# Kernel optimization log

Measured on AMD Instinct MI355X. Metric: run time of the kernel, lower is better.

The kernel has to match this reference:

```python
import jax, jax.numpy as jnp
import numpy as np

B, N = 16, 64
ATTR, STATE, REL, G = 4, 16, 9, 32
NF = 256  # nf_particle = nf_relation = nf_effect


def _mk_params(key):
    ks = jax.random.split(key, 16)
    s = 0.05
    p = {
        'enc_w0': jax.random.normal(ks[0], (ATTR + STATE, NF)) * s,
        'enc_b0': jnp.zeros((NF,)),
        'enc_w1': jax.random.normal(ks[1], (NF, NF)) * s,
        'enc_b1': jnp.zeros((NF,)),
        'rel_w0': jax.random.normal(ks[2], (REL + STATE + 2 * ATTR, NF)) * s,
        'rel_b0': jnp.zeros((NF,)),
        'rel_w1': jax.random.normal(ks[3], (NF, NF)) * s,
        'rel_b1': jnp.zeros((NF,)),
        'rp_w': jax.random.normal(ks[4], (NF + 2 * NF, NF)) * s,
        'rp_b': jnp.zeros((NF,)),
        'pp_w': jax.random.normal(ks[5], (2 * NF, NF)) * s,
        'pp_b': jnp.zeros((NF,)),
        'pred_w0': jax.random.normal(ks[6], (NF, NF)) * s,
        'pred_b0': jnp.zeros((NF,)),
        'pred_w1': jax.random.normal(ks[7], (NF, G)) * s,
        'pred_b1': jnp.zeros((G,)),
    }
    return p


def setup_inputs() -> dict:
    key = jax.random.key(0)
    k1, k2, k3, k4 = jax.random.split(key, 4)
    inp = {
        'attrs': jax.random.normal(k1, (B, N, ATTR), dtype=jnp.float32),
        'states': jax.random.normal(k2, (B, N, STATE), dtype=jnp.float32),
        'rel_attrs': jax.random.uniform(k3, (B, N, N, REL), dtype=jnp.float32),
        'pstep': 2,
    }
    inp.update(_mk_params(k4))
    return inp


def reference(attrs, states, rel_attrs,
              enc_w0, enc_b0, enc_w1, enc_b1,
              rel_w0, rel_b0, rel_w1, rel_b1,
              rp_w, rp_b, pp_w, pp_b,
              pred_w0, pred_b0, pred_w1, pred_b1,
              pstep):
    relu = jax.nn.relu
    b, n = attrs.shape[0], attrs.shape[1]

    # particle (object) encoder: ReLU(Linear) -> ReLU(Linear)
    obj_in = jnp.concatenate([attrs, states], axis=-1)          # B,N,attr+state
    obj = relu(relu(obj_in @ enc_w0 + enc_b0) @ enc_w1 + enc_b1)  # B,N,NF

    # relation encoder inputs: rel_attrs, pairwise state diffs, recv/send attrs
    rel_states = states[:, :, None, :] - states[:, None, :, :]   # B,N,N,state
    recv_attr = jnp.broadcast_to(attrs[:, :, None, :], (b, n, n, attrs.shape[-1]))
    send_attr = jnp.broadcast_to(attrs[:, None, :, :], (b, n, n, attrs.shape[-1]))
    rel_in = jnp.concatenate([rel_attrs, rel_states, recv_attr, send_attr], axis=-1)
    rel_enc = relu(relu(rel_in @ rel_w0 + rel_b0) @ rel_w1 + rel_b1)  # B,N,N,NF

    # propagation steps (small fixed count; loop over pstep is structural)
    for _ in range(pstep):
        recv = jnp.broadcast_to(obj[:, :, None, :], (b, n, n, obj.shape[-1]))
        send = jnp.broadcast_to(obj[:, None, :, :], (b, n, n, obj.shape[-1]))
        rel_eff = relu(jnp.concatenate([rel_enc, recv, send], axis=-1) @ rp_w + rp_b)
        agg = rel_eff.sum(axis=2)                                 # B,N,NF
        obj = relu(jnp.concatenate([obj, agg], axis=-1) @ pp_w + pp_b)

    # particle predictor + tanh (state encoder variant)
    out = jnp.tanh(relu(obj @ pred_w0 + pred_b0) @ pred_w1 + pred_b1)  # B,N,G
    return out
```

## Files before the change

kernel.cpp:

```cpp
#include <hip/hip_runtime.h>
#include <hip/hip_bf16.h>
#include <math.h>

#define BB 16
#define NN 64
#define ATTR 4
#define STATE 16
#define RELD 9
#define GG 32
#define NF 256
#define NROWS_OBJ (BB*NN)
#define NROWS_REL (BB*NN*NN)

typedef _Float16 half8 __attribute__((ext_vector_type(8)));
typedef _Float16 half4 __attribute__((ext_vector_type(4)));
typedef float  floatx4 __attribute__((ext_vector_type(4)));
typedef unsigned short ushort_t;

__device__ __forceinline__ void split2h(float x, _Float16& h, _Float16& l) {
  h = (_Float16)x;
  l = (_Float16)(x - (float)h);
}

#define F0_ELEMS (2 * 16 * 64 * 8)
#define F1_ELEMS (8 * 16 * 64 * 8)
#define F_TOTAL  (F0_ELEMS + 2 * F1_ELEMS)

__device__ __forceinline__ float4 gemm4_k64(const float* __restrict__ W,
                                            const float* A,
                                            int kseg, int rsel, int c4)
{
  float4 p = make_float4(0.f, 0.f, 0.f, 0.f);
  int k0 = kseg * 64;
#pragma unroll 8
  for (int k = 0; k < 64; ++k) {
    float4 w = *(const float4*)(W + (size_t)(k0 + k) * NF + c4);
    float a = A[rsel * NF + k0 + k];
    p.x += a * w.x; p.y += a * w.y; p.z += a * w.z; p.w += a * w.w;
  }
  return p;
}

__global__ __launch_bounds__(1024) void enc_qr_prep_kernel(
    const float* __restrict__ attrs, const float* __restrict__ states,
    const float* __restrict__ w0, const float* __restrict__ b0,
    const float* __restrict__ w1, const float* __restrict__ b1,
    const float* __restrict__ rpw, const float* __restrict__ rpb,
    const float* __restrict__ rel_w0, const float* __restrict__ rel_w1,
    _Float16* __restrict__ F0, _Float16* __restrict__ F1,
    _Float16* __restrict__ F2,
    float* __restrict__ obj, float* __restrict__ Q, float* __restrict__ R)
{
  int tid = threadIdx.x;
  for (int idx = blockIdx.x * 1024 + tid; idx < F_TOTAL; idx += 256 * 1024) {
    if (idx < F0_ELEMS) {
      int j = idx & 7, lane = (idx >> 3) & 63, g = (idx >> 9) & 15, s = idx >> 13;
      int k = s * 32 + (lane >> 4) * 8 + j, n = g * 16 + (lane & 15);
      float v = (k < 33) ? rel_w0[k * NF + n] : 0.f;
      F0[idx] = (_Float16)v;
    } else if (idx < F0_ELEMS + F1_ELEMS) {
      int t = idx - F0_ELEMS;
      int j = t & 7, lane = (t >> 3) & 63, g = (t >> 9) & 15, s = t >> 13;
      int k = s * 32 + (lane >> 4) * 8 + j, n = g * 16 + (lane & 15);
      F1[t] = (_Float16)rel_w1[k * NF + n];
    } else {
      int t = idx - (F0_ELEMS + F1_ELEMS);
      int j = t & 7, lane = (t >> 3) & 63, g = (t >> 9) & 15, s = t >> 13;
      int k = s * 32 + (lane >> 4) * 8 + j, n = g * 16 + (lane & 15);
      F2[t] = (_Float16)rpw[k * NF + n];
    }
  }
  __shared__ float X[4 * 20];
  __shared__ float H[4 * NF];
  __shared__ float O[4 * NF];
  __shared__ __align__(16) float red[16 * NF];
  int row0 = blockIdx.x * 4;
  if (tid < 80) {
    int r = tid / 20, k = tid % 20;
    int m = row0 + r;
    X[tid] = (k < ATTR) ? attrs[m * ATTR + k] : states[m * STATE + (k - ATTR)];
  }
  __syncthreads();
  int r = tid >> 8, c = tid & 255;
  int kseg = tid >> 8, rsel = (tid >> 6) & 3, c4 = (tid & 63) * 4;
  {
    float a = b0[c];
#pragma unroll
    for (int k = 0; k < 20; ++k) a += X[r * 20 + k] * w0[k * NF + c];
    H[r * NF + c] = fmaxf(a, 0.f);
  }
  __syncthreads();
  {
    float4 p = gemm4_k64(w1, H, kseg, rsel, c4);
    *(float4*)(&red[(kseg * 4 + rsel) * NF + c4]) = p;
  }
  __syncthreads();
  {
    float a = b1[c] + red[(0 + r) * NF + c] + red[(4 + r) * NF + c]
            + red[(8 + r) * NF + c] + red[(12 + r) * NF + c];
    a = fmaxf(a, 0.f);
    O[r * NF + c] = a;
    obj[(row0 + r) * NF + c] = a;
  }
  __syncthreads();
  {
    int gs = tid >> 9, ks2 = (tid >> 8) & 1;
    const float* W = gs ? (rpw + 512 * NF) : (rpw + 256 * NF);
    float4 p = gemm4_k64(W, O, ks2 * 2, rsel, c4);
    float4 q = gemm4_k64(W, O, ks2 * 2 + 1, rsel, c4);
    p.x += q.x; p.y += q.y; p.z += q.z; p.w += q.w;
    *(float4*)(&red[((gs * 2 + ks2) * 4 + rsel) * NF + c4]) = p;
  }
  __syncthreads();
  Q[(row0 + r) * NF + c] = rpb[c] + red[(0 + r) * NF + c] + red[(4 + r) * NF + c];
  R[(row0 + r) * NF + c] = red[(8 + r) * NF + c] + red[(12 + r) * NF + c];
}

#define ROWS 32
#define NRT 2
#define HSTR 264
#define XSTR 72

__global__ __launch_bounds__(256, 4) void rel_agg_store_mfma(
    const float* __restrict__ attrs, const float* __restrict__ states,
    const float* __restrict__ rel_attrs,
    const _Float16* __restrict__ F0, const float* __restrict__ b0,
    const _Float16* __restrict__ F1, const float* __restrict__ b1,
    const _Float16* __restrict__ F2,
    const float* __restrict__ Q, const float* __restrict__ R,
    _Float16* __restrict__ P, float* __restrict__ part)
{
  __shared__ __align__(16) _Float16 S[2 * ROWS * HSTR];
  _Float16* Hh = S;
  _Float16* Hl = S + ROWS * HSTR;
  _Float16* Xh = Hh;
  _Float16* Xl = Hl;

  int tid  = threadIdx.x;
  int wave = tid >> 6;
  int lane = tid & 63;
  int quad = lane >> 4;
  int l16  = lane & 15;
  int row0 = blockIdx.x * ROWS;

  for (int idx = tid; idx < ROWS * 64; idx += 256) {
    int r = idx >> 6, k = idx & 63;
    int grow = row0 + r;
    int j = grow & 63, i = (grow >> 6) & 63, b = grow >> 12;
    float v = 0.f;
    if (k < RELD)                     v = rel_attrs[(size_t)grow * RELD + k];
    else if (k < RELD + STATE)        v = states[(b * NN + i) * STATE + (k - RELD)]
                                        - states[(b * NN + j) * STATE + (k - RELD)];
    else if (k < RELD + STATE + ATTR) v = attrs[(b * NN + i) * ATTR + (k - RELD - STATE)];
    else if (k < 33)                  v = attrs[(b * NN + j) * ATTR + (k - RELD - STATE - ATTR)];
    _Float16 h, l; split2h(v, h, l);
    Xh[r * XSTR + k] = h;
    Xl[r * XSTR + k] = l;
  }
  __syncthreads();

  floatx4 acc[NRT][4];

#define ZERO_ACC() do { \
  _Pragma("unroll") for (int rt = 0; rt < NRT; ++rt) \
  _Pragma("unroll") for (int ct = 0; ct < 4; ++ct) acc[rt][ct] = (floatx4)(0.f); } while (0)

#define STAGE(Sn, AH, AL, ASTR, BF) do { \
  half8 ah[2][NRT], al[2][NRT], bf[2][4]; \
  _Pragma("unroll") for (int ct = 0; ct < 4; ++ct) \
    bf[0][ct] = *(const half8*)((BF) + (size_t)((wave * 4 + ct) * 64 + lane) * 8); \
  _Pragma("unroll") for (int rt = 0; rt < NRT; ++rt) { \
    ah[0][rt] = *(const half8*)(&(AH)[(rt * 16 + l16) * (ASTR) + quad * 8]); \
    al[0][rt] = *(const half8*)(&(AL)[(rt * 16 + l16) * (ASTR) + quad * 8]); } \
  _Pragma("unroll") \
  for (int s = 0; s < (Sn); ++s) { \
    int cur = s & 1, nxt = cur ^ 1; \
    if (s + 1 < (Sn)) { \
      _Pragma("unroll") for (int ct = 0; ct < 4; ++ct) \
        bf[nxt][ct] = *(const half8*)((BF) + (size_t)(((s + 1) * 16 + wave * 4 + ct) * 64 + lane) * 8); \
      _Pragma("unroll") for (int rt = 0; rt < NRT; ++rt) { \
        ah[nxt][rt] = *(const half8*)(&(AH)[(rt * 16 + l16) * (ASTR) + (s + 1) * 32 + quad * 8]); \
        al[nxt][rt] = *(const half8*)(&(AL)[(rt * 16 + l16) * (ASTR) + (s + 1) * 32 + quad * 8]); } } \
    _Pragma("unroll") for (int rt = 0; rt < NRT; ++rt) \
    _Pragma("unroll") for (int ct = 0; ct < 4; ++ct) { \
      acc[rt][ct] = __builtin_amdgcn_mfma_f32_16x16x32_f16(ah[cur][rt], bf[cur][ct], acc[rt][ct], 0, 0, 0); \
      acc[rt][ct] = __builtin_amdgcn_mfma_f32_16x16x32_f16(al[cur][rt], bf[cur][ct], acc[rt][ct], 0, 0, 0); } \
  } } while (0)

  ZERO_ACC();
  STAGE(2, Xh, Xl, XSTR, F0);
  __syncthreads();
#pragma unroll
  for (int ct = 0; ct < 4; ++ct) {
    int col = wave * 64 + ct * 16 + l16;
    float bias = b0[col];
#pragma unroll
    for (int rt = 0; rt < NRT; ++rt)
#pragma unroll
      for (int r = 0; r < 4; ++r) {
        int row = rt * 16 + quad * 4 + r;
        float h = fmaxf(acc[rt][ct][r] + bias, 0.f);
        split2h(h, Hh[row * HSTR + col], Hl[row * HSTR + col]);
      }
  }
  __syncthreads();

  ZERO_ACC();
  STAGE(8, Hh, Hl, HSTR, F1);
  __syncthreads();
#pragma unroll
  for (int ct = 0; ct < 4; ++ct) {
    int col = wave * 64 + ct * 16 + l16;
    float bias = b1[col];
#pragma unroll
    for (int rt = 0; rt < NRT; ++rt)
#pragma unroll
      for (int r = 0; r < 4; ++r) {
        int row = rt * 16 + quad * 4 + r;
        float e = fmaxf(acc[rt][ct][r] + bias, 0.f);
        split2h(e, Hh[row * HSTR + col], Hl[row * HSTR + col]);
      }
  }
  __syncthreads();

  ZERO_ACC();
  STAGE(8, Hh, Hl, HSTR, F2);

#pragma unroll
  for (int ct = 0; ct < 4; ++ct) {
    int col = wave * 64 + ct * 16 + l16;
#pragma unroll
    for (int rt = 0; rt < NRT; ++rt)
#pragma unroll
      for (int r = 0; r < 4; ++r) {
        int row = rt * 16 + quad * 4 + r;
        P[(size_t)(row0 + row) * NF + col] = (_Float16)acc[rt][ct][r];
      }
  }
  __syncthreads();

  {
    float* Rs = (float*)S;
    int bi    = row0 >> 6;
    int jbase = row0 & 63;
    int b     = row0 >> 12;
    for (int idx = tid; idx < ROWS * NF; idx += 256) {
      int rr = idx >> 8, cc = idx & 255;
      Rs[idx] = R[(size_t)(b * NN + jbase + rr) * NF + cc];
    }
    __syncthreads();
#pragma unroll
    for (int ct = 0; ct < 4; ++ct) {
      int col = wave * 64 + ct * 16 + l16;
      float q = Q[bi * NF + col];
      float s = 0.f;
#pragma unroll
      for (int rt = 0; rt < NRT; ++rt)
#pragma unroll
        for (int r = 0; r < 4; ++r) {
          int row = rt * 16 + quad * 4 + r;
          s += fmaxf(acc[rt][ct][r] + q + Rs[row * NF + col], 0.f);
        }
      s += __shfl_xor(s, 16, 64);
      s += __shfl_xor(s, 32, 64);
      if (quad == 0)
        part[((size_t)bi * 2 + (jbase >> 5)) * NF + col] = s;
    }
  }
#undef ZERO_ACC
#undef STAGE
}

__global__ __launch_bounds__(1024) void upd_qr_kernel(
    const float* __restrict__ part, const float* __restrict__ obj,
    const float* __restrict__ ppw, const float* __restrict__ ppb,
    const float* __restrict__ rpw, const float* __restrict__ rpb,
    float* __restrict__ obj_out, float* __restrict__ Qo, float* __restrict__ Ro)
{
  __shared__ float A[4 * NF];
  __shared__ float G[4 * NF];
  __shared__ __align__(16) float red[16 * NF];
  int tid = threadIdx.x;
  int row0 = blockIdx.x * 4;
  int r = tid >> 8, c = tid & 255;
  int kseg = tid >> 8, rsel = (tid >> 6) & 3, c4 = (tid & 63) * 4;
  A[r * NF + c] = obj[(row0 + r) * NF + c];
  G[r * NF + c] = part[((size_t)(row0 + r) * 2 + 0) * NF + c]
                + part[((size_t)(row0 + r) * 2 + 1) * NF + c];
  __syncthreads();
  {
    float4 p = gemm4_k64(ppw, A, kseg, rsel, c4);
    float4 q = gemm4_k64(ppw + NF * NF, G, kseg, rsel, c4);
    p.x += q.x; p.y += q.y; p.z += q.z; p.w += q.w;
    *(float4*)(&red[(kseg * 4 + rsel) * NF + c4]) = p;
  }
  __syncthreads();
  {
    float a = ppb[c] + red[(0 + r) * NF + c] + red[(4 + r) * NF + c]
            + red[(8 + r) * NF + c] + red[(12 + r) * NF + c];
    float o = fmaxf(a, 0.f);
    A[r * NF + c] = o;
    obj_out[(row0 + r) * NF + c] = o;
  }
  __syncthreads();
  {
    int gs = tid >> 9, ks2 = (tid >> 8) & 1;
    const float* W = gs ? (rpw + 512 * NF) : (rpw + 256 * NF);
    float4 p = gemm4_k64(W, A, ks2 * 2, rsel, c4);
    float4 q = gemm4_k64(W, A, ks2 * 2 + 1, rsel, c4);
    p.x += q.x; p.y += q.y; p.z += q.z; p.w += q.w;
    *(float4*)(&red[((gs * 2 + ks2) * 4 + rsel) * NF + c4]) = p;
  }
  __syncthreads();
  Qo[(row0 + r) * NF + c] = rpb[c] + red[(0 + r) * NF + c] + red[(4 + r) * NF + c];
  Ro[(row0 + r) * NF + c] = red[(8 + r) * NF + c] + red[(12 + r) * NF + c];
}

__global__ __launch_bounds__(1024) void aggupd_pred_kernel(
    const _Float16* __restrict__ P, const float* __restrict__ Q,
    const float* __restrict__ R, const float* __restrict__ obj,
    const float* __restrict__ ppw, const float* __restrict__ ppb,
    const float* __restrict__ w0, const float* __restrict__ b0,
    const float* __restrict__ w1, const float* __restrict__ b1,
    float* __restrict__ out)
{
  __shared__ float A[4 * NF];
  __shared__ float G[4 * NF];
  __shared__ __align__(16) float red[16 * NF];
  int tid = threadIdx.x;
  int row0 = blockIdx.x * 4;
  int b = row0 >> 6;
  int r = tid >> 8, c = tid & 255;
  int kseg = tid >> 8, rsel = (tid >> 6) & 3, c4 = (tid & 63) * 4;
  {
    int rr = (tid >> 6) & 3;
    int jq = tid >> 8;
    float4 q4 = *(const float4*)(Q + (row0 + rr) * NF + c4);
    const _Float16* Pb = P + ((size_t)(row0 + rr) * NN + jq * 16) * NF + c4;
    const float* Rb = R + (size_t)(b * NN + jq * 16) * NF + c4;
    float4 s = make_float4(0.f, 0.f, 0.f, 0.f);
#pragma unroll
    for (int j = 0; j < 16; ++j) {
      half4 ph  = *(const half4*)(Pb + (size_t)j * NF);
      float4 rv = *(const float4*)(Rb + (size_t)j * NF);
      s.x += fmaxf((float)ph[0] + q4.x + rv.x, 0.f);
      s.y += fmaxf((float)ph[1] + q4.y + rv.y, 0.f);
      s.z += fmaxf((float)ph[2] + q4.z + rv.z, 0.f);
      s.w += fmaxf((float)ph[3] + q4.w + rv.w, 0.f);
    }
    *(float4*)(&red[(jq * 4 + rr) * NF + c4]) = s;
    A[r * NF + c] = obj[(row0 + r) * NF + c];
  }
  __syncthreads();
  G[r * NF + c] = red[(0 + r) * NF + c] + red[(4 + r) * NF + c]
                + red[(8 + r) * NF + c] + red[(12 + r) * NF + c];
  __syncthreads();
  {
    float4 p = gemm4_k64(ppw, A, kseg, rsel, c4);
    float4 q = gemm4_k64(ppw + NF * NF, G, kseg, rsel, c4);
    p.x += q.x; p.y += q.y; p.z += q.z; p.w += q.w;
    *(float4*)(&red[(kseg * 4 + rsel) * NF + c4]) = p;
  }
  __syncthreads();
  {
    float a = ppb[c] + red[(0 + r) * NF + c] + red[(4 + r) * NF + c]
            + red[(8 + r) * NF + c] + red[(12 + r) * NF + c];
    A[r * NF + c] = fmaxf(a, 0.f);
  }
  __syncthreads();
  {
    float4 p = gemm4_k64(w0, A, kseg, rsel, c4);
    *(float4*)(&red[(kseg * 4 + rsel) * NF + c4]) = p;
  }
  __syncthreads();
  {
    float a = b0[c] + red[(0 + r) * NF + c] + red[(4 + r) * NF + c]
            + red[(8 + r) * NF + c] + red[(12 + r) * NF + c];
    G[r * NF + c] = fmaxf(a, 0.f);
  }
  __syncthreads();
  {
    int ks8 = tid >> 7, rr = (tid >> 5) & 3, g = tid & 31;
    float s = 0.f;
#pragma unroll 8
    for (int k = 0; k < 32; ++k)
      s += G[rr * NF + ks8 * 32 + k] * w1[(ks8 * 32 + k) * GG + g];
    red[tid] = s;
  }
  __syncthreads();
  if (tid < 4 * GG) {
    int rr = tid >> 5, g = tid & 31;
    float a = b1[g];
#pragma unroll
    for (int ks = 0; ks < 8; ++ks) a += red[ks * 128 + tid];
    out[(row0 + rr) * GG + g] = tanhf(a);
  }
}

extern "C" void kernel_launch(void* const* d_in, const int* in_sizes, int n_in,
                              void* d_out, int out_size, void* d_ws, size_t ws_size,
                              hipStream_t stream)
{
  const float* attrs     = (const float*)d_in[0];
  const float* states    = (const float*)d_in[1];
  const float* rel_attrs = (const float*)d_in[2];
  const float* enc_w0  = (const float*)d_in[4];
  const float* enc_b0  = (const float*)d_in[5];
  const float* enc_w1  = (const float*)d_in[6];
  const float* enc_b1  = (const float*)d_in[7];
  const float* rel_w0  = (const float*)d_in[8];
  const float* rel_b0  = (const float*)d_in[9];
  const float* rel_w1  = (const float*)d_in[10];
  const float* rel_b1  = (const float*)d_in[11];
  const float* rp_w    = (const float*)d_in[12];
  const float* rp_b    = (const float*)d_in[13];
  const float* pp_w    = (const float*)d_in[14];
  const float* pp_b    = (const float*)d_in[15];
  const float* pred_w0 = (const float*)d_in[16];
  const float* pred_b0 = (const float*)d_in[17];
  const float* pred_w1 = (const float*)d_in[18];
  const float* pred_b1 = (const float*)d_in[19];
  float* out = (float*)d_out;

  char* ws = (char*)d_ws;
  _Float16* P  = (_Float16*)ws;
  float* obj0  = (float*)(ws + (size_t)NROWS_REL * NF * sizeof(_Float16));
  float* obj1  = obj0 + NROWS_OBJ * NF;
  float* Q0    = obj1 + NROWS_OBJ * NF;
  float* R0    = Q0 + NROWS_OBJ * NF;
  float* Q1    = R0 + NROWS_OBJ * NF;
  float* R1    = Q1 + NROWS_OBJ * NF;
  float* part1 = R1 + NROWS_OBJ * NF;
  _Float16* F0 = (_Float16*)(part1 + 2 * (size_t)NROWS_OBJ * NF);
  _Float16* F1 = F0 + F0_ELEMS;
  _Float16* F2 = F1 + F1_ELEMS;

  enc_qr_prep_kernel<<<NROWS_OBJ / 4, 1024, 0, stream>>>(
      attrs, states, enc_w0, enc_b0, enc_w1, enc_b1, rp_w, rp_b,
      rel_w0, rel_w1, F0, F1, F2, obj0, Q0, R0);
  rel_agg_store_mfma<<<NROWS_REL / ROWS, 256, 0, stream>>>(
      attrs, states, rel_attrs,
      F0, rel_b0, F1, rel_b1, F2,
      Q0, R0, P, part1);
  upd_qr_kernel<<<NROWS_OBJ / 4, 1024, 0, stream>>>(part1, obj0, pp_w, pp_b,
                                                    rp_w, rp_b, obj1, Q1, R1);
  aggupd_pred_kernel<<<NROWS_OBJ / 4, 1024, 0, stream>>>(P, Q1, R1, obj1,
                                                         pp_w, pp_b,
                                                         pred_w0, pred_b0,
                                                         pred_w1, pred_b1, out);
}
```

Before: 231.2 us.

## Swizzle hidden-activation LDS layout to drop padding and raise occupancy

Removes the row padding from the shared hidden-activation buffer (stride 264 to 256) and applies an XOR swizzle on the column index so that MFMA operand reads and epilogue writes stay free of bank conflicts. The smaller LDS footprint supports raising the launch bound from 4 to 5 blocks per SM. It also wraps the MFMA issue block in s_setprio to favour matrix instructions among competing waves. The risk is register pressure under the tighter launch bound, which could cause spills, and any other code that reads the hidden buffer must use the same swizzle.

```diff
diff --git a/kernel.cpp b/kernel.cpp
--- a/kernel.cpp
+++ b/kernel.cpp
@@ -118,10 +118,14 @@
 
 #define ROWS 32
 #define NRT 2
-#define HSTR 264
+#define HSTR 256
 #define XSTR 72
 
-__global__ __launch_bounds__(256, 4) void rel_agg_store_mfma(
+__device__ __forceinline__ int hsw(int row, int col) {
+  return ((row << 8) + col) ^ (((row >> 1) & 7) << 3);
+}
+
+__global__ __launch_bounds__(256, 5) void rel_agg_store_mfma(
     const float* __restrict__ attrs, const float* __restrict__ states,
     const float* __restrict__ rel_attrs,
     const _Float16* __restrict__ F0, const float* __restrict__ b0,
@@ -165,13 +169,15 @@
   _Pragma("unroll") for (int rt = 0; rt < NRT; ++rt) \
   _Pragma("unroll") for (int ct = 0; ct < 4; ++ct) acc[rt][ct] = (floatx4)(0.f); } while (0)
 
-#define STAGE(Sn, AH, AL, ASTR, BF) do { \
+#define STAGE(Sn, AH, AL, ASTR, SW, BF) do { \
   half8 ah[2][NRT], al[2][NRT], bf[2][4]; \
   _Pragma("unroll") for (int ct = 0; ct < 4; ++ct) \
     bf[0][ct] = *(const half8*)((BF) + (size_t)((wave * 4 + ct) * 64 + lane) * 8); \
   _Pragma("unroll") for (int rt = 0; rt < NRT; ++rt) { \
-    ah[0][rt] = *(const half8*)(&(AH)[(rt * 16 + l16) * (ASTR) + quad * 8]); \
-    al[0][rt] = *(const half8*)(&(AL)[(rt * 16 + l16) * (ASTR) + quad * 8]); } \
+    int ao = (rt * 16 + l16) * (ASTR) + quad * 8; \
+    if (SW) ao ^= ((l16 >> 1) & 7) << 3; \
+    ah[0][rt] = *(const half8*)(&(AH)[ao]); \
+    al[0][rt] = *(const half8*)(&(AL)[ao]); } \
   _Pragma("unroll") \
   for (int s = 0; s < (Sn); ++s) { \
     int cur = s & 1, nxt = cur ^ 1; \
@@ -179,16 +185,20 @@
       _Pragma("unroll") for (int ct = 0; ct < 4; ++ct) \
         bf[nxt][ct] = *(const half8*)((BF) + (size_t)(((s + 1) * 16 + wave * 4 + ct) * 64 + lane) * 8); \
       _Pragma("unroll") for (int rt = 0; rt < NRT; ++rt) { \
-        ah[nxt][rt] = *(const half8*)(&(AH)[(rt * 16 + l16) * (ASTR) + (s + 1) * 32 + quad * 8]); \
-        al[nxt][rt] = *(const half8*)(&(AL)[(rt * 16 + l16) * (ASTR) + (s + 1) * 32 + quad * 8]); } } \
+        int ao = (rt * 16 + l16) * (ASTR) + (s + 1) * 32 + quad * 8; \
+        if (SW) ao ^= ((l16 >> 1) & 7) << 3; \
+        ah[nxt][rt] = *(const half8*)(&(AH)[ao]); \
+        al[nxt][rt] = *(const half8*)(&(AL)[ao]); } } \
+    __builtin_amdgcn_s_setprio(1); \
     _Pragma("unroll") for (int rt = 0; rt < NRT; ++rt) \
     _Pragma("unroll") for (int ct = 0; ct < 4; ++ct) { \
       acc[rt][ct] = __builtin_amdgcn_mfma_f32_16x16x32_f16(ah[cur][rt], bf[cur][ct], acc[rt][ct], 0, 0, 0); \
       acc[rt][ct] = __builtin_amdgcn_mfma_f32_16x16x32_f16(al[cur][rt], bf[cur][ct], acc[rt][ct], 0, 0, 0); } \
+    __builtin_amdgcn_s_setprio(0); \
   } } while (0)
 
   ZERO_ACC();
-  STAGE(2, Xh, Xl, XSTR, F0);
+  STAGE(2, Xh, Xl, XSTR, 0, F0);
   __syncthreads();
 #pragma unroll
   for (int ct = 0; ct < 4; ++ct) {
@@ -200,13 +210,14 @@
       for (int r = 0; r < 4; ++r) {
         int row = rt * 16 + quad * 4 + r;
         float h = fmaxf(acc[rt][ct][r] + bias, 0.f);
-        split2h(h, Hh[row * HSTR + col], Hl[row * HSTR + col]);
+        int o = hsw(row, col);
+        split2h(h, Hh[o], Hl[o]);
       }
   }
   __syncthreads();
 
   ZERO_ACC();
-  STAGE(8, Hh, Hl, HSTR, F1);
+  STAGE(8, Hh, Hl, HSTR, 1, F1);
   __syncthreads();
 #pragma unroll
   for (int ct = 0; ct < 4; ++ct) {
@@ -218,13 +229,14 @@
       for (int r = 0; r < 4; ++r) {
         int row = rt * 16 + quad * 4 + r;
         float e = fmaxf(acc[rt][ct][r] + bias, 0.f);
-        split2h(e, Hh[row * HSTR + col], Hl[row * HSTR + col]);
+        int o = hsw(row, col);
+        split2h(e, Hh[o], Hl[o]);
       }
   }
   __syncthreads();
 
   ZERO_ACC();
-  STAGE(8, Hh, Hl, HSTR, F2);
+  STAGE(8, Hh, Hl, HSTR, 1, F2);
 
 #pragma unroll
   for (int ct = 0; ct < 4; ++ct) {
```

Measured after the change: 427.6 us. 1.85x slower.

## Retile small object GEMMs into 32-row tiles split across more kernels

Applied to the files above, without the earlier changes.

Replaces the 4-row-per-block fused object-side kernels (encoder+QR, update+QR, aggregation+update+predictor) with separate kernels that each compute a 32-row by 32-column tile with a 4-way K split. Each weight element fetched from global memory is now reused across 32 rows instead of 4, which cuts weight traffic for the small fp32 GEMMs. The cost is several more kernel launches and intermediate round trips through global memory (G2, T, obj2). The weight-fragment prep loop now relies on the grid covering F_TOTAL in a single pass.

```diff
diff --git a/kernel.cpp b/kernel.cpp
--- a/kernel.cpp
+++ b/kernel.cpp
@@ -15,7 +15,6 @@
 typedef _Float16 half8 __attribute__((ext_vector_type(8)));
 typedef _Float16 half4 __attribute__((ext_vector_type(4)));
 typedef float  floatx4 __attribute__((ext_vector_type(4)));
-typedef unsigned short ushort_t;
 
 __device__ __forceinline__ void split2h(float x, _Float16& h, _Float16& l) {
   h = (_Float16)x;
@@ -26,33 +25,44 @@
 #define F1_ELEMS (8 * 16 * 64 * 8)
 #define F_TOTAL  (F0_ELEMS + 2 * F1_ELEMS)
 
-__device__ __forceinline__ float4 gemm4_k64(const float* __restrict__ W,
-                                            const float* A,
-                                            int kseg, int rsel, int c4)
-{
-  float4 p = make_float4(0.f, 0.f, 0.f, 0.f);
-  int k0 = kseg * 64;
-#pragma unroll 8
-  for (int k = 0; k < 64; ++k) {
-    float4 w = *(const float4*)(W + (size_t)(k0 + k) * NF + c4);
-    float a = A[rsel * NF + k0 + k];
-    p.x += a * w.x; p.y += a * w.y; p.z += a * w.z; p.w += a * w.w;
-  }
-  return p;
-}
-
-__global__ __launch_bounds__(1024) void enc_qr_prep_kernel(
+
+__device__ __forceinline__ floatx4 tile_part(const float* __restrict__ W, int ws,
+                                             const float* A, int as,
+                                             int kbase, int nq, int r, int col)
+{
+  floatx4 acc = (floatx4)(0.f);
+#pragma unroll 4
+  for (int q = 0; q < nq; ++q) {
+    int kk = kbase + q * 4;
+    floatx4 a4 = *(const floatx4*)(A + r * as + kk);
+    acc += a4[0] * *(const floatx4*)(W + (size_t)(kk + 0) * ws + col);
+    acc += a4[1] * *(const floatx4*)(W + (size_t)(kk + 1) * ws + col);
+    acc += a4[2] * *(const floatx4*)(W + (size_t)(kk + 2) * ws + col);
+    acc += a4[3] * *(const floatx4*)(W + (size_t)(kk + 3) * ws + col);
+  }
+  return acc;
+}
+
+__device__ __forceinline__ floatx4 relu4(floatx4 v) {
+  v[0] = fmaxf(v[0], 0.f); v[1] = fmaxf(v[1], 0.f);
+  v[2] = fmaxf(v[2], 0.f); v[3] = fmaxf(v[3], 0.f);
+  return v;
+}
+
+#define RED4(ks, rr, cc) (*(const floatx4*)(&red[(((ks)*32+(rr))*8+(cc))*4]))
+
+__global__ __launch_bounds__(1024) void enc_obj_kernel(
     const float* __restrict__ attrs, const float* __restrict__ states,
     const float* __restrict__ w0, const float* __restrict__ b0,
     const float* __restrict__ w1, const float* __restrict__ b1,
-    const float* __restrict__ rpw, const float* __restrict__ rpb,
+    const float* __restrict__ rpw,
     const float* __restrict__ rel_w0, const float* __restrict__ rel_w1,
     _Float16* __restrict__ F0, _Float16* __restrict__ F1,
-    _Float16* __restrict__ F2,
-    float* __restrict__ obj, float* __restrict__ Q, float* __restrict__ R)
-{
-  int tid = threadIdx.x;
-  for (int idx = blockIdx.x * 1024 + tid; idx < F_TOTAL; idx += 256 * 1024) {
+    _Float16* __restrict__ F2, float* __restrict__ obj)
+{
+  int tid = threadIdx.x;
+  {
+    int idx = blockIdx.x * 1024 + tid;
     if (idx < F0_ELEMS) {
       int j = idx & 7, lane = (idx >> 3) & 63, g = (idx >> 9) & 15, s = idx >> 13;
       int k = s * 32 + (lane >> 4) * 8 + j, n = g * 16 + (lane & 15);
@@ -63,57 +73,214 @@
       int j = t & 7, lane = (t >> 3) & 63, g = (t >> 9) & 15, s = t >> 13;
       int k = s * 32 + (lane >> 4) * 8 + j, n = g * 16 + (lane & 15);
       F1[t] = (_Float16)rel_w1[k * NF + n];
-    } else {
+    } else if (idx < F_TOTAL) {
       int t = idx - (F0_ELEMS + F1_ELEMS);
       int j = t & 7, lane = (t >> 3) & 63, g = (t >> 9) & 15, s = t >> 13;
       int k = s * 32 + (lane >> 4) * 8 + j, n = g * 16 + (lane & 15);
       F2[t] = (_Float16)rpw[k * NF + n];
     }
   }
-  __shared__ float X[4 * 20];
-  __shared__ float H[4 * NF];
-  __shared__ float O[4 * NF];
-  __shared__ __align__(16) float red[16 * NF];
-  int row0 = blockIdx.x * 4;
-  if (tid < 80) {
-    int r = tid / 20, k = tid % 20;
-    int m = row0 + r;
-    X[tid] = (k < ATTR) ? attrs[m * ATTR + k] : states[m * STATE + (k - ATTR)];
-  }
-  __syncthreads();
-  int r = tid >> 8, c = tid & 255;
-  int kseg = tid >> 8, rsel = (tid >> 6) & 3, c4 = (tid & 63) * 4;
-  {
-    float a = b0[c];
-#pragma unroll
-    for (int k = 0; k < 20; ++k) a += X[r * 20 + k] * w0[k * NF + c];
-    H[r * NF + c] = fmaxf(a, 0.f);
-  }
-  __syncthreads();
-  {
-    float4 p = gemm4_k64(w1, H, kseg, rsel, c4);
-    *(float4*)(&red[(kseg * 4 + rsel) * NF + c4]) = p;
-  }
-  __syncthreads();
-  {
-    float a = b1[c] + red[(0 + r) * NF + c] + red[(4 + r) * NF + c]
-            + red[(8 + r) * NF + c] + red[(12 + r) * NF + c];
-    a = fmaxf(a, 0.f);
-    O[r * NF + c] = a;
-    obj[(row0 + r) * NF + c] = a;
-  }
-  __syncthreads();
-  {
-    int gs = tid >> 9, ks2 = (tid >> 8) & 1;
-    const float* W = gs ? (rpw + 512 * NF) : (rpw + 256 * NF);
-    float4 p = gemm4_k64(W, O, ks2 * 2, rsel, c4);
-    float4 q = gemm4_k64(W, O, ks2 * 2 + 1, rsel, c4);
-    p.x += q.x; p.y += q.y; p.z += q.z; p.w += q.w;
-    *(float4*)(&red[((gs * 2 + ks2) * 4 + rsel) * NF + c4]) = p;
-  }
-  __syncthreads();
-  Q[(row0 + r) * NF + c] = rpb[c] + red[(0 + r) * NF + c] + red[(4 + r) * NF + c];
-  R[(row0 + r) * NF + c] = red[(8 + r) * NF + c] + red[(12 + r) * NF + c];
+  __shared__ float X[32 * 20];
+  __shared__ __align__(16) float H[32 * 260];
+  __shared__ __align__(16) float red[4096];
+  int mt = blockIdx.x >> 3, nt = blockIdx.x & 7;
+  int row0 = mt * 32;
+  for (int idx = tid; idx < 32 * 20; idx += 1024) {
+    int rr = idx / 20, k = idx % 20;
+    int m = row0 + rr;
+    X[idx] = (k < ATTR) ? attrs[m * ATTR + k] : states[m * STATE + (k - ATTR)];
+  }
+  __syncthreads();
+  for (int idx = tid; idx < 2048; idx += 1024) {
+    int rr = idx >> 6, cc = (idx & 63) * 4;
+    floatx4 a = *(const floatx4*)(b0 + cc);
+#pragma unroll
+    for (int k = 0; k < 20; ++k)
+      a += X[rr * 20 + k] * *(const floatx4*)(w0 + k * NF + cc);
+    *(floatx4*)(H + rr * 260 + cc) = relu4(a);
+  }
+  __syncthreads();
+  int kseg = tid >> 8, r = (tid >> 3) & 31, cg = tid & 7;
+  int col = nt * 32 + cg * 4;
+  floatx4 acc = tile_part(w1, NF, H, 260, kseg * 64, 16, r, col);
+  *(floatx4*)(&red[((kseg * 32 + r) * 8 + cg) * 4]) = acc;
+  __syncthreads();
+  if (tid < 256) {
+    int rr = tid >> 3, cc = tid & 7;
+    int col2 = nt * 32 + cc * 4;
+    floatx4 s = RED4(0, rr, cc) + RED4(1, rr, cc) + RED4(2, rr, cc) + RED4(3, rr, cc)
+              + *(const floatx4*)(b1 + col2);
+    *(floatx4*)(obj + (size_t)(row0 + rr) * NF + col2) = relu4(s);
+  }
+}
+
+__global__ __launch_bounds__(1024) void qr_kernel(
+    const float* __restrict__ objp, const float* __restrict__ rpw,
+    const float* __restrict__ rpb,
+    float* __restrict__ Qo, float* __restrict__ Ro)
+{
+  __shared__ __align__(16) float A[32 * 260];
+  __shared__ __align__(16) float red[4096];
+  int tid = threadIdx.x;
+  int mt = blockIdx.x >> 4, nt = blockIdx.x & 15;
+  int row0 = mt * 32;
+  for (int idx = tid; idx < 2048; idx += 1024) {
+    int rr = idx >> 6, q = idx & 63;
+    *(floatx4*)(A + rr * 260 + q * 4) =
+        *(const floatx4*)(objp + (size_t)(row0 + rr) * NF + q * 4);
+  }
+  __syncthreads();
+  int kseg = tid >> 8, r = (tid >> 3) & 31, cg = tid & 7;
+  int col512 = nt * 32 + cg * 4;
+  const float* W = (nt < 8) ? (rpw + 256 * NF) : (rpw + 512 * NF);
+  int wcol = (nt < 8) ? col512 : (col512 - 256);
+  floatx4 acc = tile_part(W, NF, A, 260, kseg * 64, 16, r, wcol);
+  *(floatx4*)(&red[((kseg * 32 + r) * 8 + cg) * 4]) = acc;
+  __syncthreads();
+  if (tid < 256) {
+    int rr = tid >> 3, cc = tid & 7;
+    int c512 = nt * 32 + cc * 4;
+    floatx4 s = RED4(0, rr, cc) + RED4(1, rr, cc) + RED4(2, rr, cc) + RED4(3, rr, cc);
+    if (nt < 8) {
+      s += *(const floatx4*)(rpb + c512);
+      *(floatx4*)(Qo + (size_t)(row0 + rr) * NF + c512) = s;
+    } else {
+      *(floatx4*)(Ro + (size_t)(row0 + rr) * NF + (c512 - 256)) = s;
+    }
+  }
+}
+
+__global__ __launch_bounds__(1024) void upd_kernel(
+    const float* __restrict__ objp, const float* __restrict__ gA, int gsum2,
+    const float* __restrict__ ppw, const float* __restrict__ ppb,
+    float* __restrict__ obj_out)
+{
+  __shared__ __align__(16) float A[32 * 516];
+  __shared__ __align__(16) float red[4096];
+  int tid = threadIdx.x;
+  int mt = blockIdx.x >> 3, nt = blockIdx.x & 7;
+  int row0 = mt * 32;
+  for (int idx = tid; idx < 4096; idx += 1024) {
+    int rr = idx >> 7, q = idx & 127;
+    floatx4 v;
+    if (q < 64) {
+      v = *(const floatx4*)(objp + (size_t)(row0 + rr) * NF + q * 4);
+    } else {
+      int cc = (q - 64) * 4;
+      if (gsum2)
+        v = *(const floatx4*)(gA + ((size_t)(row0 + rr) * 2) * NF + cc)
+          + *(const floatx4*)(gA + ((size_t)(row0 + rr) * 2 + 1) * NF + cc);
+      else
+        v = *(const floatx4*)(gA + (size_t)(row0 + rr) * NF + cc);
+    }
+    *(floatx4*)(A + rr * 516 + q * 4) = v;
+  }
+  __syncthreads();
+  int kseg = tid >> 8, r = (tid >> 3) & 31, cg = tid & 7;
+  int col = nt * 32 + cg * 4;
+  floatx4 acc = tile_part(ppw, NF, A, 516, kseg * 128, 32, r, col);
+  *(floatx4*)(&red[((kseg * 32 + r) * 8 + cg) * 4]) = acc;
+  __syncthreads();
+  if (tid < 256) {
+    int rr = tid >> 3, cc = tid & 7;
+    int col2 = nt * 32 + cc * 4;
+    floatx4 s = RED4(0, rr, cc) + RED4(1, rr, cc) + RED4(2, rr, cc) + RED4(3, rr, cc)
+              + *(const floatx4*)(ppb + col2);
+    *(floatx4*)(obj_out + (size_t)(row0 + rr) * NF + col2) = relu4(s);
+  }
+}
+
+__global__ __launch_bounds__(1024) void aggsweep_kernel(
+    const _Float16* __restrict__ P, const float* __restrict__ Q1,
+    const float* __restrict__ R1, float* __restrict__ G2)
+{
+  __shared__ __align__(16) float red[4096];
+  int tid = threadIdx.x;
+  int mt = blockIdx.x >> 3, nt = blockIdx.x & 7;
+  int row0 = mt * 32;
+  int b = row0 >> 6;
+  int jseg = tid >> 8, r = (tid >> 3) & 31, cg = tid & 7;
+  int col = nt * 32 + cg * 4;
+  int i = row0 + r;
+  floatx4 q4 = *(const floatx4*)(Q1 + (size_t)i * NF + col);
+  const _Float16* Pb = P + ((size_t)i * NN + jseg * 16) * NF + col;
+  const float* Rb = R1 + ((size_t)(b * NN) + jseg * 16) * NF + col;
+  floatx4 s = (floatx4)(0.f);
+#pragma unroll
+  for (int j = 0; j < 16; ++j) {
+    half4 ph = *(const half4*)(Pb + (size_t)j * NF);
+    floatx4 rv = *(const floatx4*)(Rb + (size_t)j * NF);
+    s[0] += fmaxf((float)ph[0] + q4[0] + rv[0], 0.f);
+    s[1] += fmaxf((float)ph[1] + q4[1] + rv[1], 0.f);
+    s[2] += fmaxf((float)ph[2] + q4[2] + rv[2], 0.f);
+    s[3] += fmaxf((float)ph[3] + q4[3] + rv[3], 0.f);
+  }
+  *(floatx4*)(&red[((jseg * 32 + r) * 8 + cg) * 4]) = s;
+  __syncthreads();
+  if (tid < 256) {
+    int rr = tid >> 3, cc = tid & 7;
+    int col2 = nt * 32 + cc * 4;
+    floatx4 g = RED4(0, rr, cc) + RED4(1, rr, cc) + RED4(2, rr, cc) + RED4(3, rr, cc);
+    *(floatx4*)(G2 + (size_t)(row0 + rr) * NF + col2) = g;
+  }
+}
+
+__global__ __launch_bounds__(1024) void lin256_kernel(
+    const float* __restrict__ Ain, const float* __restrict__ W,
+    const float* __restrict__ bias, float* __restrict__ outp)
+{
+  __shared__ __align__(16) float A[32 * 260];
+  __shared__ __align__(16) float red[4096];
+  int tid = threadIdx.x;
+  int mt = blockIdx.x >> 3, nt = blockIdx.x & 7;
+  int row0 = mt * 32;
+  for (int idx = tid; idx < 2048; idx += 1024) {
+    int rr = idx >> 6, q = idx & 63;
+    *(floatx4*)(A + rr * 260 + q * 4) =
+        *(const floatx4*)(Ain + (size_t)(row0 + rr) * NF + q * 4);
+  }
+  __syncthreads();
+  int kseg = tid >> 8, r = (tid >> 3) & 31, cg = tid & 7;
+  int col = nt * 32 + cg * 4;
+  floatx4 acc = tile_part(W, NF, A, 260, kseg * 64, 16, r, col);
+  *(floatx4*)(&red[((kseg * 32 + r) * 8 + cg) * 4]) = acc;
+  __syncthreads();
+  if (tid < 256) {
+    int rr = tid >> 3, cc = tid & 7;
+    int col2 = nt * 32 + cc * 4;
+    floatx4 s = RED4(0, rr, cc) + RED4(1, rr, cc) + RED4(2, rr, cc) + RED4(3, rr, cc)
+              + *(const floatx4*)(bias + col2);
+    *(floatx4*)(outp + (size_t)(row0 + rr) * NF + col2) = relu4(s);
+  }
+}
+
+__global__ __launch_bounds__(1024) void pred2_kernel(
+    const float* __restrict__ T, const float* __restrict__ w1,
+    const float* __restrict__ b1, float* __restrict__ outp)
+{
+  __shared__ __align__(16) float A[32 * 260];
+  __shared__ __align__(16) float red[4096];
+  int tid = threadIdx.x;
+  int row0 = blockIdx.x * 32;
+  for (int idx = tid; idx < 2048; idx += 1024) {
+    int rr = idx >> 6, q = idx & 63;
+    *(floatx4*)(A + rr * 260 + q * 4) =
+        *(const floatx4*)(T + (size_t)(row0 + rr) * NF + q * 4);
+  }
+  __syncthreads();
+  int kseg = tid >> 8, r = (tid >> 3) & 31, cg = tid & 7;
+  int col = cg * 4;
+  floatx4 acc = tile_part(w1, GG, A, 260, kseg * 64, 16, r, col);
+  *(floatx4*)(&red[((kseg * 32 + r) * 8 + cg) * 4]) = acc;
+  __syncthreads();
+  if (tid < 256) {
+    int rr = tid >> 3, cc = tid & 7;
+    int col2 = cc * 4;
+    floatx4 s = RED4(0, rr, cc) + RED4(1, rr, cc) + RED4(2, rr, cc) + RED4(3, rr, cc)
+              + *(const floatx4*)(b1 + col2);
+    s[0] = tanhf(s[0]); s[1] = tanhf(s[1]); s[2] = tanhf(s[2]); s[3] = tanhf(s[3]);
+    *(floatx4*)(outp + (size_t)(row0 + rr) * GG + col2) = s;
+  }
 }
 
 #define ROWS 32
@@ -271,132 +438,6 @@
 #undef STAGE
 }
 
-__global__ __launch_bounds__(1024) void upd_qr_kernel(
-    const float* __restrict__ part, const float* __restrict__ obj,
-    const float* __restrict__ ppw, const float* __restrict__ ppb,
-    const float* __restrict__ rpw, const float* __restrict__ rpb,
-    float* __restrict__ obj_out, float* __restrict__ Qo, float* __restrict__ Ro)
-{
-  __shared__ float A[4 * NF];
-  __shared__ float G[4 * NF];
-  __shared__ __align__(16) float red[16 * NF];
-  int tid = threadIdx.x;
-  int row0 = blockIdx.x * 4;
-  int r = tid >> 8, c = tid & 255;
-  int kseg = tid >> 8, rsel = (tid >> 6) & 3, c4 = (tid & 63) * 4;
-  A[r * NF + c] = obj[(row0 + r) * NF + c];
-  G[r * NF + c] = part[((size_t)(row0 + r) * 2 + 0) * NF + c]
-                + part[((size_t)(row0 + r) * 2 + 1) * NF + c];
-  __syncthreads();
-  {
-    float4 p = gemm4_k64(ppw, A, kseg, rsel, c4);
-    float4 q = gemm4_k64(ppw + NF * NF, G, kseg, rsel, c4);
-    p.x += q.x; p.y += q.y; p.z += q.z; p.w += q.w;
-    *(float4*)(&red[(kseg * 4 + rsel) * NF + c4]) = p;
-  }
-  __syncthreads();
-  {
-    float a = ppb[c] + red[(0 + r) * NF + c] + red[(4 + r) * NF + c]
-            + red[(8 + r) * NF + c] + red[(12 + r) * NF + c];
-    float o = fmaxf(a, 0.f);
-    A[r * NF + c] = o;
-    obj_out[(row0 + r) * NF + c] = o;
-  }
-  __syncthreads();
-  {
-    int gs = tid >> 9, ks2 = (tid >> 8) & 1;
-    const float* W = gs ? (rpw + 512 * NF) : (rpw + 256 * NF);
-    float4 p = gemm4_k64(W, A, ks2 * 2, rsel, c4);
-    float4 q = gemm4_k64(W, A, ks2 * 2 + 1, rsel, c4);
-    p.x += q.x; p.y += q.y; p.z += q.z; p.w += q.w;
-    *(float4*)(&red[((gs * 2 + ks2) * 4 + rsel) * NF + c4]) = p;
-  }
-  __syncthreads();
-  Qo[(row0 + r) * NF + c] = rpb[c] + red[(0 + r) * NF + c] + red[(4 + r) * NF + c];
-  Ro[(row0 + r) * NF + c] = red[(8 + r) * NF + c] + red[(12 + r) * NF + c];
-}
-
-__global__ __launch_bounds__(1024) void aggupd_pred_kernel(
-    const _Float16* __restrict__ P, const float* __restrict__ Q,
-    const float* __restrict__ R, const float* __restrict__ obj,
-    const float* __restrict__ ppw, const float* __restrict__ ppb,
-    const float* __restrict__ w0, const float* __restrict__ b0,
-    const float* __restrict__ w1, const float* __restrict__ b1,
-    float* __restrict__ out)
-{
-  __shared__ float A[4 * NF];
-  __shared__ float G[4 * NF];
-  __shared__ __align__(16) float red[16 * NF];
-  int tid = threadIdx.x;
-  int row0 = blockIdx.x * 4;
-  int b = row0 >> 6;
-  int r = tid >> 8, c = tid & 255;
-  int kseg = tid >> 8, rsel = (tid >> 6) & 3, c4 = (tid & 63) * 4;
-  {
-    int rr = (tid >> 6) & 3;
-    int jq = tid >> 8;
-    float4 q4 = *(const float4*)(Q + (row0 + rr) * NF + c4);
-    const _Float16* Pb = P + ((size_t)(row0 + rr) * NN + jq * 16) * NF + c4;
-    const float* Rb = R + (size_t)(b * NN + jq * 16) * NF + c4;
-    float4 s = make_float4(0.f, 0.f, 0.f, 0.f);
-#pragma unroll
-    for (int j = 0; j < 16; ++j) {
-      half4 ph  = *(const half4*)(Pb + (size_t)j * NF);
-      float4 rv = *(const float4*)(Rb + (size_t)j * NF);
-      s.x += fmaxf((float)ph[0] + q4.x + rv.x, 0.f);
-      s.y += fmaxf((float)ph[1] + q4.y + rv.y, 0.f);
-      s.z += fmaxf((float)ph[2] + q4.z + rv.z, 0.f);
-      s.w += fmaxf((float)ph[3] + q4.w + rv.w, 0.f);
-    }
-    *(float4*)(&red[(jq * 4 + rr) * NF + c4]) = s;
-    A[r * NF + c] = obj[(row0 + r) * NF + c];
-  }
-  __syncthreads();
-  G[r * NF + c] = red[(0 + r) * NF + c] + red[(4 + r) * NF + c]
-                + red[(8 + r) * NF + c] + red[(12 + r) * NF + c];
-  __syncthreads();
-  {
-    float4 p = gemm4_k64(ppw, A, kseg, rsel, c4);
-    float4 q = gemm4_k64(ppw + NF * NF, G, kseg, rsel, c4);
-    p.x += q.x; p.y += q.y; p.z += q.z; p.w += q.w;
-    *(float4*)(&red[(kseg * 4 + rsel) * NF + c4]) = p;
-  }
-  __syncthreads();
-  {
-    float a = ppb[c] + red[(0 + r) * NF + c] + red[(4 + r) * NF + c]
-            + red[(8 + r) * NF + c] + red[(12 + r) * NF + c];
-    A[r * NF + c] = fmaxf(a, 0.f);
-  }
-  __syncthreads();
-  {
-    float4 p = gemm4_k64(w0, A, kseg, rsel, c4);
-    *(float4*)(&red[(kseg * 4 + rsel) * NF + c4]) = p;
-  }
-  __syncthreads();
-  {
-    float a = b0[c] + red[(0 + r) * NF + c] + red[(4 + r) * NF + c]
-            + red[(8 + r) * NF + c] + red[(12 + r) * NF + c];
-    G[r * NF + c] = fmaxf(a, 0.f);
-  }
-  __syncthreads();
-  {
-    int ks8 = tid >> 7, rr = (tid >> 5) & 3, g = tid & 31;
-    float s = 0.f;
-#pragma unroll 8
-    for (int k = 0; k < 32; ++k)
-      s += G[rr * NF + ks8 * 32 + k] * w1[(ks8 * 32 + k) * GG + g];
-    red[tid] = s;
-  }
-  __syncthreads();
-  if (tid < 4 * GG) {
-    int rr = tid >> 5, g = tid & 31;
-    float a = b1[g];
-#pragma unroll
-    for (int ks = 0; ks < 8; ++ks) a += red[ks * 128 + tid];
-    out[(row0 + rr) * GG + g] = tanhf(a);
-  }
-}
-
 extern "C" void kernel_launch(void* const* d_in, const int* in_sizes, int n_in,
                               void* d_out, int out_size, void* d_ws, size_t ws_size,
                               hipStream_t stream)
@@ -434,18 +475,22 @@
   _Float16* F0 = (_Float16*)(part1 + 2 * (size_t)NROWS_OBJ * NF);
   _Float16* F1 = F0 + F0_ELEMS;
   _Float16* F2 = F1 + F1_ELEMS;
-
-  enc_qr_prep_kernel<<<NROWS_OBJ / 4, 1024, 0, stream>>>(
-      attrs, states, enc_w0, enc_b0, enc_w1, enc_b1, rp_w, rp_b,
-      rel_w0, rel_w1, F0, F1, F2, obj0, Q0, R0);
+  float* G2   = part1;
+  float* obj2 = obj0;
+  float* T    = Q0;
+
+  enc_obj_kernel<<<256, 1024, 0, stream>>>(
+      attrs, states, enc_w0, enc_b0, enc_w1, enc_b1, rp_w,
+      rel_w0, rel_w1, F0, F1, F2, obj0);
+  qr_kernel<<<512, 1024, 0, stream>>>(obj0, rp_w, rp_b, Q0, R0);
   rel_agg_store_mfma<<<NROWS_REL / ROWS, 256, 0, stream>>>(
       attrs, states, rel_attrs,
       F0, rel_b0, F1, rel_b1, F2,
       Q0, R0, P, part1);
-  upd_qr_kernel<<<NROWS_OBJ / 4, 1024, 0, stream>>>(part1, obj0, pp_w, pp_b,
-                                                    rp_w, rp_b, obj1, Q1, R1);
-  aggupd_pred_kernel<<<NROWS_OBJ / 4, 1024, 0, stream>>>(P, Q1, R1, obj1,
-                                                         pp_w, pp_b,
-                                                         pred_w0, pred_b0,
-                                                         pred_w1, pred_b1, out);
-}
+  upd_kernel<<<256, 1024, 0, stream>>>(obj0, part1, 1, pp_w, pp_b, obj1);
+  qr_kernel<<<512, 1024, 0, stream>>>(obj1, rp_w, rp_b, Q1, R1);
+  aggsweep_kernel<<<256, 1024, 0, stream>>>(P, Q1, R1, G2);
+  upd_kernel<<<256, 1024, 0, stream>>>(obj1, G2, 0, pp_w, pp_b, obj2);
+  lin256_kernel<<<256, 1024, 0, stream>>>(obj2, pred_w0, pred_b0, T);
+  pred2_kernel<<<32, 1024, 0, stream>>>(T, pred_w1, pred_b1, out);
+}
```

Result: slower. 258.9 us (+12.0%).
